# Performance work log

Measured on AMD Instinct MI355X. Metric: run time of the kernel, lower is better.

The kernel has to match this reference:

```python
import jax, jax.numpy as jnp
import numpy as np

N_HEAD = 16
N_KV_HEAD = 4
WINDOW = 256
ROPE_BASE = 10000.0


def _rotate_half(x):
    h = x.shape[-1] // 2
    return jnp.concatenate([-x[..., h:], x[..., :h]], axis=-1)


def _rope_cos_sin(T, D):
    inv_freq = 1.0 / (ROPE_BASE ** (jnp.arange(0, D, 2, dtype=jnp.float32) / D))
    t = jnp.arange(T, dtype=jnp.float32)
    freqs = t[:, None] * inv_freq[None, :]            # [T, D/2]
    emb = jnp.concatenate([freqs, freqs], axis=-1)    # [T, D]
    return jnp.cos(emb)[None, None], jnp.sin(emb)[None, None]  # [1,1,T,D]


def _masks(T, w):
    tq = jnp.arange(T)
    tk = jnp.arange(T)
    causal = tk[None, :] <= tq[:, None]
    i_blk = (tq // w) * w                              # window block start per query
    k_start = jnp.maximum(0, i_blk - w // 2)           # local key slice start
    # torch SDPA is_causal with L!=S: top-left aligned tril -> local kj <= local qi
    upper = tq - (i_blk - k_start)
    local = (tk[None, :] >= k_start[:, None]) & (tk[None, :] <= upper[:, None])
    return causal, local


def setup_inputs() -> dict:
    key = jax.random.key(0)
    k0, k1, k2, k3, k4 = jax.random.split(key, 5)
    B, T, C = 1, 2048, 2048
    D = C // N_HEAD
    s = 0.02
    return {
        "x": jax.random.normal(k0, (B, T, C), dtype=jnp.float32),
        "wq": jax.random.normal(k1, (C, N_HEAD * D), dtype=jnp.float32) * s,
        "wk": jax.random.normal(k2, (C, N_KV_HEAD * D), dtype=jnp.float32) * s,
        "wv": jax.random.normal(k3, (C, N_KV_HEAD * D), dtype=jnp.float32) * s,
        "wo": jax.random.normal(k4, (C, C), dtype=jnp.float32) * s,
    }


def reference(x, wq, wk, wv, wo):
    B, T, C = x.shape
    D = C // N_HEAD
    g = N_HEAD // N_KV_HEAD

    q = (x @ wq).reshape(B, T, N_HEAD, D)
    k = (x @ wk).reshape(B, T, N_KV_HEAD, D)
    v = (x @ wv).reshape(B, T, N_KV_HEAD, D)
    k = jnp.repeat(k, g, axis=2)                       # GQA repeat_interleave
    v = jnp.repeat(v, g, axis=2)
    q = q.transpose(0, 2, 1, 3)                        # [B,H,T,D]
    k = k.transpose(0, 2, 1, 3)
    v = v.transpose(0, 2, 1, 3)

    cos, sin = _rope_cos_sin(T, D)
    q = q * cos + _rotate_half(q) * sin
    k = k * cos + _rotate_half(k) * sin

    scale = 1.0 / jnp.sqrt(jnp.asarray(D, dtype=q.dtype))
    scores = jnp.einsum('bhqd,bhkd->bhqk', q, k) * scale
    causal, local = _masks(T, WINDOW)
    neg = jnp.finfo(scores.dtype).min
    p_g = jax.nn.softmax(jnp.where(causal, scores, neg), axis=-1)
    p_l = jax.nn.softmax(jnp.where(local, scores, neg), axis=-1)
    out_g = jnp.einsum('bhqk,bhkd->bhqd', p_g, v)
    out_l = jnp.einsum('bhqk,bhkd->bhqd', p_l, v)
    out = 0.5 * (out_g + out_l)
    out = out.transpose(0, 2, 1, 3).reshape(B, T, C)
    return out @ wo
```

## Files before the change

### kernel.cpp

```cpp
#include <hip/hip_runtime.h>
#include <hip/hip_bf16.h>
#include <cstdint>
#include <cstddef>

#define T_SEQ 2048
#define CDIM  2048
#define HQ    16
#define HKV   4
#define DHEAD 128
#define NQKV  3072

typedef __bf16 bf8 __attribute__((ext_vector_type(8)));
typedef __bf16 bf4 __attribute__((ext_vector_type(4)));
typedef float  f4  __attribute__((ext_vector_type(4)));

static __device__ __forceinline__ f4 mfma16(bf8 a, bf8 b, f4 c) {
    return __builtin_amdgcn_mfma_f32_16x16x32_bf16(a, b, c, 0, 0, 0);
}

#define GLOAD16(g, l)                                                        \
    __builtin_amdgcn_global_load_lds(                                        \
        (const __attribute__((address_space(1))) void*)(g),                  \
        (__attribute__((address_space(3))) void*)(l), 16, 0, 0)

__global__ __launch_bounds__(256) void k_prep(const float* __restrict__ in,
                                              __bf16* __restrict__ out,
                                              float* __restrict__ tab) {
    const int bid = blockIdx.x;
    if (bid < 4096) {
        int i = bid * 256 + threadIdx.x;
        float4 v = ((const float4*)in)[i];
        bf4 o;
        o[0] = (__bf16)v.x; o[1] = (__bf16)v.y; o[2] = (__bf16)v.z; o[3] = (__bf16)v.w;
        ((bf4*)out)[i] = o;
    } else {
        int idx = (bid - 4096) * 256 + threadIdx.x;
        int t = idx >> 6, j = idx & 63;
        float invf = expf(-(float)j * (9.210340371976184f / 64.0f));
        float a = (float)t * invf;
        tab[idx * 2 + 0] = cosf(a);
        tab[idx * 2 + 1] = sinf(a);
    }
}

__global__ __launch_bounds__(256) void k_tpose4(const float* __restrict__ wq,
                                                const float* __restrict__ wk,
                                                const float* __restrict__ wv,
                                                const float* __restrict__ wo,
                                                __bf16* __restrict__ wqkvT,
                                                __bf16* __restrict__ woT) {
    __shared__ float tile[32][33];
    const int bx = blockIdx.x;
    const float* src; __bf16* dst; int ld_src, cx;
    if (bx < 64)      { src = wq; dst = wqkvT;                        ld_src = 2048; cx = bx; }
    else if (bx < 80) { src = wk; dst = wqkvT + (size_t)2048 * 2048;  ld_src = 512;  cx = bx - 64; }
    else if (bx < 96) { src = wv; dst = wqkvT + (size_t)2560 * 2048;  ld_src = 512;  cx = bx - 80; }
    else              { src = wo; dst = woT;                          ld_src = 2048; cx = bx - 96; }
    const int c0 = cx * 32, r0 = blockIdx.y * 32;
    const int tx = threadIdx.x, ty = threadIdx.y;
#pragma unroll
    for (int i = 0; i < 4; ++i)
        tile[ty + i * 8][tx] = src[(size_t)(r0 + ty + i * 8) * ld_src + c0 + tx];
    __syncthreads();
#pragma unroll
    for (int i = 0; i < 4; ++i)
        dst[(size_t)(c0 + ty + i * 8) * 2048 + r0 + tx] = (__bf16)tile[tx][ty + i * 8];
}

template <int MODE>
__global__ __launch_bounds__(256, 2) void k_gemm(const __bf16* __restrict__ A,
                                                 const __bf16* __restrict__ BT,
                                                 float* __restrict__ C,
                                                 const float2* __restrict__ tab,
                                                 __bf16* __restrict__ Qo,
                                                 __bf16* __restrict__ Ko,
                                                 __bf16* __restrict__ Vo,
                                                 int M, int N, int K) {
    __shared__ __bf16 lds[2][2][128 * 64];
    char* L = (char*)&lds[0][0][0];
    const int tid = threadIdx.x, wid = tid >> 6, lane = tid & 63;
    const int l15 = lane & 15, lhi = lane >> 4;
    const int wr = wid >> 1, wc = wid & 1;
    const size_t arow0 = (size_t)blockIdx.y * 128;
    const size_t brow0 = (size_t)blockIdx.x * 128;

    const int sr = tid >> 3;
    const int sc8 = ((tid & 7) ^ ((tid >> 3) & 7)) * 8;
    const __bf16* Ag = A + (arow0 + sr) * K + sc8;
    const __bf16* Bg = BT + (brow0 + sr) * K + sc8;

#define GSTAGE(buf, k0)                                                          \
    {                                                                            \
        _Pragma("unroll") for (int i = 0; i < 4; ++i) {                          \
            GLOAD16(Ag + (k0) + (size_t)i * 32 * K,                              \
                    L + (buf) * 32768 + i * 4096 + tid * 16);                    \
            GLOAD16(Bg + (k0) + (size_t)i * 32 * K,                              \
                    L + (buf) * 32768 + 16384 + i * 4096 + tid * 16);            \
        }                                                                        \
    }

    f4 acc[4][4] = {};
    GSTAGE(0, 0);
    __syncthreads();
    int cur = 0;

    for (int k0 = 0; k0 < K; k0 += 64) {
        if (k0 + 64 < K) GSTAGE(cur ^ 1, k0 + 64);
        const char* Ab = L + cur * 32768;
        const char* Bb = Ab + 16384;
        bf8 af[2][4], bfr[2][4];
#pragma unroll
        for (int kk = 0; kk < 2; ++kk) {
            const int ch = ((kk * 4 + lhi) ^ (l15 & 7)) * 16;
#pragma unroll
            for (int m = 0; m < 4; ++m)
                af[kk][m] = *(const bf8*)(Ab + (wr * 64 + m * 16 + l15) * 128 + ch);
#pragma unroll
            for (int n = 0; n < 4; ++n)
                bfr[kk][n] = *(const bf8*)(Bb + (n * 32 + wc * 16 + l15) * 128 + ch);
        }
        __builtin_amdgcn_s_setprio(1);
#pragma unroll
        for (int kk = 0; kk < 2; ++kk)
#pragma unroll
            for (int m = 0; m < 4; ++m)
#pragma unroll
                for (int n = 0; n < 4; ++n)
                    acc[m][n] = mfma16(af[kk][m], bfr[kk][n], acc[m][n]);
        __builtin_amdgcn_s_setprio(0);
        __syncthreads();
        cur ^= 1;
    }
#undef GSTAGE

    const int row0 = blockIdx.y * 128 + wr * 64;
    if (MODE == 0) {
#pragma unroll
        for (int m = 0; m < 4; ++m)
#pragma unroll
            for (int n = 0; n < 4; ++n) {
                const int c = blockIdx.x * 128 + n * 32 + wc * 16 + l15;
#pragma unroll
                for (int j = 0; j < 4; ++j)
                    C[(size_t)(row0 + m * 16 + lhi * 4 + j) * N + c] = acc[m][n][j];
            }
    } else {
        const int bx = blockIdx.x;
        if (bx < 20) {
            __bf16* dst0 = (bx < 16) ? (Qo + (size_t)bx * T_SEQ * DHEAD)
                                     : (Ko + (size_t)(bx - 16) * T_SEQ * DHEAD);
#pragma unroll
            for (int m = 0; m < 4; ++m)
#pragma unroll
                for (int n = 0; n < 2; ++n) {
                    const int d = n * 32 + wc * 16 + l15;
#pragma unroll
                    for (int j = 0; j < 4; ++j) {
                        const int t = row0 + m * 16 + lhi * 4 + j;
                        const float2 cs = tab[t * 64 + d];
                        const float a = acc[m][n][j], b = acc[m][n + 2][j];
                        dst0[(size_t)t * DHEAD + d]      = (__bf16)(a * cs.x - b * cs.y);
                        dst0[(size_t)t * DHEAD + d + 64] = (__bf16)(b * cs.x + a * cs.y);
                    }
                }
        } else {
            __bf16* vdst = Vo + (size_t)(bx - 20) * DHEAD * T_SEQ;
#pragma unroll
            for (int m = 0; m < 4; ++m)
#pragma unroll
                for (int n = 0; n < 4; ++n) {
                    const int c = n * 32 + wc * 16 + l15;
                    bf4 o;
#pragma unroll
                    for (int j = 0; j < 4; ++j) o[j] = (__bf16)acc[m][n][j];
                    *(bf4*)&vdst[(size_t)c * T_SEQ + row0 + m * 16 + lhi * 4] = o;
                }
        }
    }
}

__global__ __launch_bounds__(512) void k_attn(const __bf16* __restrict__ Q,
                                              const __bf16* __restrict__ Kr,
                                              const __bf16* __restrict__ VT,
                                              __bf16* __restrict__ att) {
    __shared__ __align__(16) char lds[155648];
    char* KlB  = lds;
    char* VlB  = lds + 65536;
    char* PlB0 = lds + 131072;
    char* PwB0 = lds + 147456;

    const int h = blockIdx.y, kvh = h >> 2;
    const int qt = (blockIdx.y < 8) ? (31 - (int)blockIdx.x) : (int)blockIdx.x;
    const int tid = threadIdx.x, wid = tid >> 6, lane = tid & 63;
    const int l15 = lane & 15, lhi = lane >> 4;
    const int par = wid >> 2, qw = wid & 3;
    const int q0w = qt * 64 + qw * 16;
    const bool hasloc = qt >= 4;
    const int lfLo = 4 * (qt >> 2) - 2;
    const int lpart = qt - 2;
    const float CE = 0.12751741f;
    const float L2E = 1.44269504f;
    const float SCL = 0.08838834764831845f;
    const float THR = 5.5451774f;

    char* PlB = PlB0 + wid * 2048;
    char* PwB = PwB0 + qw * 2048;

    const int srow = tid >> 4;
    const int sg = (((tid & 15) ^ (srow & 15)) << 3);
    const __bf16* KgB = Kr + (size_t)kvh * T_SEQ * DHEAD;
    const __bf16* VgB = VT + (size_t)kvh * DHEAD * T_SEQ;

#define STAGE(bsel, kb2)                                                          \
    {                                                                             \
        _Pragma("unroll") for (int i = 0; i < 4; ++i) {                           \
            GLOAD16(KgB + (size_t)((kb2) + i * 32 + srow) * DHEAD + sg,           \
                    KlB + (bsel) + i * 8192 + tid * 16);                          \
            GLOAD16(VgB + (size_t)(i * 32 + srow) * T_SEQ + (kb2) + sg,           \
                    VlB + (bsel) + i * 8192 + tid * 16);                          \
        }                                                                         \
    }

    bf8 qf[4];
#pragma unroll
    for (int dc = 0; dc < 4; ++dc)
        qf[dc] = *(const bf8*)&Q[((size_t)h * T_SEQ + q0w + l15) * DHEAD + dc * 32 + lhi * 8];

    f4 oc[8] = {}, ow[8] = {};
    float mg[4], sgp[4], slp[4];
#pragma unroll
    for (int j = 0; j < 4; ++j) { mg[j] = -__builtin_inff(); sgp[j] = slp[j] = 0.f; }
    float mgmin = -__builtin_inff();

    const int R = (qt >> 1) + 1;
    STAGE(0, 0);
    __syncthreads();
    int cur = 0;

    for (int r = 0; r < R; ++r) {
        if (r + 1 < R) STAGE((cur ^ 1) * 32768, (r + 1) * 128);
        const int kt = 2 * r + par;
        if (kt <= qt) {
            const int kb = kt * 64;
            const int cb = cur * 32768;
            const int rowb = par * 64;
            f4 sc[4] = {};
            __builtin_amdgcn_s_setprio(1);
#pragma unroll
            for (int ks = 0; ks < 4; ++ks)
#pragma unroll
                for (int dc = 0; dc < 4; ++dc) {
                    bf8 kf = *(const bf8*)(KlB + cb + (rowb + ks * 16 + l15) * 256 +
                                           (((dc * 4 + lhi) ^ l15) << 4));
                    sc[ks] = mfma16(qf[dc], kf, sc[ks]);
                }
            __builtin_amdgcn_s_setprio(0);

            float t[4][4];
#pragma unroll
            for (int ks = 0; ks < 4; ++ks)
#pragma unroll
                for (int j = 0; j < 4; ++j) t[ks][j] = sc[ks][j];
            if (kt == qt) {
#pragma unroll
                for (int ks = 0; ks < 4; ++ks)
#pragma unroll
                    for (int j = 0; j < 4; ++j)
                        if (kb + ks * 16 + l15 > q0w + lhi * 4 + j) t[ks][j] = -3.0e38f;
            }
            float mx = t[0][0];
#pragma unroll
            for (int ks = 0; ks < 4; ++ks)
#pragma unroll
                for (int j = 0; j < 4; ++j) mx = fmaxf(mx, t[ks][j]);
            mx *= SCL;
            if (!__all(mx <= mgmin + THR)) {
#pragma unroll
                for (int j = 0; j < 4; ++j) {
                    float m2 = fmaxf(fmaxf(t[0][j], t[1][j]), fmaxf(t[2][j], t[3][j])) * SCL;
#pragma unroll
                    for (int x = 1; x < 16; x <<= 1) m2 = fmaxf(m2, __shfl_xor(m2, x));
                    float mn = fmaxf(mg[j], m2);
                    float f = __builtin_amdgcn_exp2f((mg[j] - mn) * L2E);
                    mg[j] = mn;
                    sgp[j] *= f; slp[j] *= f;
#pragma unroll
                    for (int nd = 0; nd < 8; ++nd) { oc[nd][j] *= f; ow[nd][j] *= f; }
                }
                mgmin = fminf(fminf(mg[0], mg[1]), fminf(mg[2], mg[3]));
            }
            float p[4][4], psum[4];
#pragma unroll
            for (int j = 0; j < 4; ++j) {
                const float bj = mg[j] * L2E;
#pragma unroll
                for (int ks = 0; ks < 4; ++ks)
                    p[ks][j] = __builtin_amdgcn_exp2f(t[ks][j] * CE - bj);
                psum[j] = (p[0][j] + p[1][j]) + (p[2][j] + p[3][j]);
                sgp[j] += psum[j];
            }
            const bool part = hasloc && (kt == lpart);
            if (!part) {
#pragma unroll
                for (int j = 0; j < 4; ++j) {
                    const int rsw = ((lhi * 4 + j) & 7) << 4;
                    const int rb = (lhi * 4 + j) * 128;
#pragma unroll
                    for (int ks = 0; ks < 4; ++ks)
                        *(__bf16*)(PlB + rb + ((ks * 32 + 2 * l15) ^ rsw)) = (__bf16)p[ks][j];
                }
            } else {
                const int e = q0w + lhi * 4 - 128 - kb - l15;
#pragma unroll
                for (int j = 0; j < 4; ++j) {
                    const int rsw = ((lhi * 4 + j) & 7) << 4;
                    const int rb = (lhi * 4 + j) * 128;
                    float lsum = 0.f;
#pragma unroll
                    for (int ks = 0; ks < 4; ++ks) {
                        float l = (ks * 16 <= e + j) ? p[ks][j] : 0.f;
                        lsum += l;
                        *(__bf16*)(PwB + rb + ((ks * 32 + 2 * l15) ^ rsw)) = (__bf16)l;
                        *(__bf16*)(PlB + rb + ((ks * 32 + 2 * l15) ^ rsw)) = (__bf16)(p[ks][j] - l);
                    }
                    slp[j] += lsum;
                }
            }
            const bool inwin = hasloc && kt >= lfLo && kt < lpart;
            if (inwin) {
#pragma unroll
                for (int j = 0; j < 4; ++j) slp[j] += psum[j];
            }
            const int psw = (l15 & 7) << 4;
            bf8 pf0 = *(const bf8*)(PlB + l15 * 128 + ((lhi << 4) ^ psw));
            bf8 pf1 = *(const bf8*)(PlB + l15 * 128 + ((64 + (lhi << 4)) ^ psw));
            const int vg0 = ((par * 8 + lhi) ^ l15) << 4;
            const int vg1 = ((par * 8 + 4 + lhi) ^ l15) << 4;
            __builtin_amdgcn_s_setprio(1);
            if (part) {
                bf8 pw0 = *(const bf8*)(PwB + l15 * 128 + ((lhi << 4) ^ psw));
                bf8 pw1 = *(const bf8*)(PwB + l15 * 128 + ((64 + (lhi << 4)) ^ psw));
#pragma unroll
                for (int nd = 0; nd < 8; ++nd) {
                    bf8 v0 = *(const bf8*)(VlB + cb + (nd * 16 + l15) * 256 + vg0);
                    bf8 v1 = *(const bf8*)(VlB + cb + (nd * 16 + l15) * 256 + vg1);
                    oc[nd] = mfma16(pf0, v0, oc[nd]);
                    oc[nd] = mfma16(pf1, v1, oc[nd]);
                    ow[nd] = mfma16(pw0, v0, ow[nd]);
                    ow[nd] = mfma16(pw1, v1, ow[nd]);
                }
            } else if (inwin) {
#pragma unroll
                for (int nd = 0; nd < 8; ++nd) {
                    bf8 v0 = *(const bf8*)(VlB + cb + (nd * 16 + l15) * 256 + vg0);
                    bf8 v1 = *(const bf8*)(VlB + cb + (nd * 16 + l15) * 256 + vg1);
                    ow[nd] = mfma16(pf0, v0, ow[nd]);
                    ow[nd] = mfma16(pf1, v1, ow[nd]);
                }
            } else {
#pragma unroll
                for (int nd = 0; nd < 8; ++nd) {
                    bf8 v0 = *(const bf8*)(VlB + cb + (nd * 16 + l15) * 256 + vg0);
                    bf8 v1 = *(const bf8*)(VlB + cb + (nd * 16 + l15) * 256 + vg1);
                    oc[nd] = mfma16(pf0, v0, oc[nd]);
                    oc[nd] = mfma16(pf1, v1, oc[nd]);
                }
            }
            __builtin_amdgcn_s_setprio(0);
        }
        __syncthreads();
        cur ^= 1;
    }

    if (par) {
        char* sb = lds + qw * 20480 + lane * 320;
#pragma unroll
        for (int nd = 0; nd < 8; ++nd) *(f4*)(sb + nd * 16) = oc[nd];
#pragma unroll
        for (int nd = 0; nd < 8; ++nd) *(f4*)(sb + 128 + nd * 16) = ow[nd];
        f4 a, b, c;
#pragma unroll
        for (int j = 0; j < 4; ++j) { a[j] = mg[j]; b[j] = sgp[j]; c[j] = slp[j]; }
        *(f4*)(sb + 256) = a; *(f4*)(sb + 272) = b; *(f4*)(sb + 288) = c;
    }
    __syncthreads();
    if (!par) {
        char* sb = lds + qw * 20480 + lane * 320;
        f4 mB = *(const f4*)(sb + 256);
        f4 sB = *(const f4*)(sb + 272);
        f4 lB = *(const f4*)(sb + 288);
        float fA[4], fB[4];
#pragma unroll
        for (int j = 0; j < 4; ++j) {
            float ms = fmaxf(mg[j], mB[j]);
            fA[j] = __builtin_amdgcn_exp2f((mg[j] - ms) * L2E);
            fB[j] = __builtin_amdgcn_exp2f((mB[j] - ms) * L2E);
            sgp[j] = sgp[j] * fA[j] + sB[j] * fB[j];
            slp[j] = slp[j] * fA[j] + lB[j] * fB[j];
        }
#pragma unroll
        for (int nd = 0; nd < 8; ++nd) {
            f4 ocB = *(const f4*)(sb + nd * 16);
            f4 owB = *(const f4*)(sb + 128 + nd * 16);
#pragma unroll
            for (int j = 0; j < 4; ++j) {
                oc[nd][j] = oc[nd][j] * fA[j] + ocB[j] * fB[j];
                ow[nd][j] = ow[nd][j] * fA[j] + owB[j] * fB[j];
            }
        }
#pragma unroll
        for (int j = 0; j < 4; ++j) {
#pragma unroll
            for (int x = 1; x < 16; x <<= 1) {
                sgp[j] += __shfl_xor(sgp[j], x);
                slp[j] += __shfl_xor(slp[j], x);
            }
        }
        float rg[4], rl[4];
#pragma unroll
        for (int j = 0; j < 4; ++j) {
            rg[j] = 1.f / sgp[j];
            rl[j] = hasloc ? 0.5f / slp[j] : 0.f;
        }
#pragma unroll
        for (int nd = 0; nd < 8; ++nd)
#pragma unroll
            for (int j = 0; j < 4; ++j) {
                int q = q0w + lhi * 4 + j;
                float go = oc[nd][j] + ow[nd][j];
                float v = hasloc ? (go * (0.5f * rg[j]) + ow[nd][j] * rl[j]) : go * rg[j];
                att[(size_t)q * CDIM + h * DHEAD + nd * 16 + l15] = (__bf16)v;
            }
    }
#undef STAGE
}

extern "C" void kernel_launch(void* const* d_in, const int* in_sizes, int n_in,
                              void* d_out, int out_size, void* d_ws, size_t ws_size,
                              hipStream_t stream) {
    const float* x  = (const float*)d_in[0];
    const float* wq = (const float*)d_in[1];
    const float* wk = (const float*)d_in[2];
    const float* wv = (const float*)d_in[3];
    const float* wo = (const float*)d_in[4];
    char* ws = (char*)d_ws;

    __bf16* xbf   = (__bf16*)(ws + 0);
    __bf16* wqkvT = (__bf16*)(ws + 8388608);
    __bf16* woT   = (__bf16*)(ws + 20971520);
    __bf16* Q     = (__bf16*)(ws + 41943040);
    __bf16* K     = (__bf16*)(ws + 50331648);
    __bf16* VTb   = (__bf16*)(ws + 52428800);
    __bf16* att   = (__bf16*)(ws + 54525952);
    float*  tab   = (float*)(ws + 62914560);

    k_prep<<<4608, 256, 0, stream>>>(x, xbf, tab);
    k_tpose4<<<dim3(160, 64), dim3(32, 8), 0, stream>>>(wq, wk, wv, wo, wqkvT, woT);
    k_gemm<1><<<dim3(24, 16), 256, 0, stream>>>(xbf, wqkvT, nullptr, (const float2*)tab,
                                                Q, K, VTb, 2048, 3072, 2048);
    k_attn<<<dim3(32, 16), 512, 0, stream>>>(Q, K, VTb, att);
    k_gemm<0><<<dim3(16, 16), 256, 0, stream>>>(att, woT, (float*)d_out, nullptr,
                                                nullptr, nullptr, nullptr, 2048, 2048, 2048);
}
```

Measured before the change: 140.2 us.

## Use eight waves per GEMM tile and merge prep and weight-transpose kernels

The GEMM block grows from 256 to 512 threads. Each of the eight waves now computes a 32x64 sub-tile of the 128x128 output instead of 64x64, and the global-to-LDS staging loop is reshaped to match. The aim is to raise waves per CU and hide more latency, since the grids are small relative to the CU count; the cost is fewer MFMAs per LDS fragment load per wave. Separately, the x/bf16 conversion, RoPE table and weight transpose kernels become one launch with block-index dispatch, removing a kernel launch and its gap.

Measured after the change: 138.1 us, median of 2. No clear change (-1.5%).

```diff
diff --git a/kernel.cpp b/kernel.cpp
--- a/kernel.cpp
+++ b/kernel.cpp
@@ -23,41 +23,43 @@
         (const __attribute__((address_space(1))) void*)(g),                  \
         (__attribute__((address_space(3))) void*)(l), 16, 0, 0)
 
-__global__ __launch_bounds__(256) void k_prep(const float* __restrict__ in,
-                                              __bf16* __restrict__ out,
-                                              float* __restrict__ tab) {
-    const int bid = blockIdx.x;
+__global__ __launch_bounds__(256) void k_pre(const float* __restrict__ x,
+                                             const float* __restrict__ wq,
+                                             const float* __restrict__ wk,
+                                             const float* __restrict__ wv,
+                                             const float* __restrict__ wo,
+                                             __bf16* __restrict__ xbf,
+                                             float* __restrict__ tab,
+                                             __bf16* __restrict__ wqkvT,
+                                             __bf16* __restrict__ woT) {
+    const int bid = blockIdx.x, tid = threadIdx.x;
     if (bid < 4096) {
-        int i = bid * 256 + threadIdx.x;
-        float4 v = ((const float4*)in)[i];
+        int i = bid * 256 + tid;
+        float4 v = ((const float4*)x)[i];
         bf4 o;
         o[0] = (__bf16)v.x; o[1] = (__bf16)v.y; o[2] = (__bf16)v.z; o[3] = (__bf16)v.w;
-        ((bf4*)out)[i] = o;
-    } else {
-        int idx = (bid - 4096) * 256 + threadIdx.x;
+        ((bf4*)xbf)[i] = o;
+        return;
+    }
+    if (bid < 4608) {
+        int idx = (bid - 4096) * 256 + tid;
         int t = idx >> 6, j = idx & 63;
         float invf = expf(-(float)j * (9.210340371976184f / 64.0f));
         float a = (float)t * invf;
         tab[idx * 2 + 0] = cosf(a);
         tab[idx * 2 + 1] = sinf(a);
-    }
-}
-
-__global__ __launch_bounds__(256) void k_tpose4(const float* __restrict__ wq,
-                                                const float* __restrict__ wk,
-                                                const float* __restrict__ wv,
-                                                const float* __restrict__ wo,
-                                                __bf16* __restrict__ wqkvT,
-                                                __bf16* __restrict__ woT) {
+        return;
+    }
     __shared__ float tile[32][33];
-    const int bx = blockIdx.x;
+    const int n = bid - 4608;
+    const int bx = n % 160, by = n / 160;
     const float* src; __bf16* dst; int ld_src, cx;
     if (bx < 64)      { src = wq; dst = wqkvT;                        ld_src = 2048; cx = bx; }
     else if (bx < 80) { src = wk; dst = wqkvT + (size_t)2048 * 2048;  ld_src = 512;  cx = bx - 64; }
     else if (bx < 96) { src = wv; dst = wqkvT + (size_t)2560 * 2048;  ld_src = 512;  cx = bx - 80; }
     else              { src = wo; dst = woT;                          ld_src = 2048; cx = bx - 96; }
-    const int c0 = cx * 32, r0 = blockIdx.y * 32;
-    const int tx = threadIdx.x, ty = threadIdx.y;
+    const int c0 = cx * 32, r0 = by * 32;
+    const int tx = tid & 31, ty = tid >> 5;
 #pragma unroll
     for (int i = 0; i < 4; ++i)
         tile[ty + i * 8][tx] = src[(size_t)(r0 + ty + i * 8) * ld_src + c0 + tx];
@@ -68,7 +70,7 @@
 }
 
 template <int MODE>
-__global__ __launch_bounds__(256, 2) void k_gemm(const __bf16* __restrict__ A,
+__global__ __launch_bounds__(512, 4) void k_gemm(const __bf16* __restrict__ A,
                                                  const __bf16* __restrict__ BT,
                                                  float* __restrict__ C,
                                                  const float2* __restrict__ tab,
@@ -91,15 +93,15 @@
 
 #define GSTAGE(buf, k0)                                                          \
     {                                                                            \
-        _Pragma("unroll") for (int i = 0; i < 4; ++i) {                          \
-            GLOAD16(Ag + (k0) + (size_t)i * 32 * K,                              \
-                    L + (buf) * 32768 + i * 4096 + tid * 16);                    \
-            GLOAD16(Bg + (k0) + (size_t)i * 32 * K,                              \
-                    L + (buf) * 32768 + 16384 + i * 4096 + tid * 16);            \
+        _Pragma("unroll") for (int i = 0; i < 2; ++i) {                          \
+            GLOAD16(Ag + (k0) + (size_t)i * 64 * K,                              \
+                    L + (buf) * 32768 + i * 8192 + tid * 16);                    \
+            GLOAD16(Bg + (k0) + (size_t)i * 64 * K,                              \
+                    L + (buf) * 32768 + 16384 + i * 8192 + tid * 16);            \
         }                                                                        \
     }
 
-    f4 acc[4][4] = {};
+    f4 acc[2][4] = {};
     GSTAGE(0, 0);
     __syncthreads();
     int cur = 0;
@@ -108,13 +110,13 @@
         if (k0 + 64 < K) GSTAGE(cur ^ 1, k0 + 64);
         const char* Ab = L + cur * 32768;
         const char* Bb = Ab + 16384;
-        bf8 af[2][4], bfr[2][4];
+        bf8 af[2][2], bfr[2][4];
 #pragma unroll
         for (int kk = 0; kk < 2; ++kk) {
             const int ch = ((kk * 4 + lhi) ^ (l15 & 7)) * 16;
 #pragma unroll
-            for (int m = 0; m < 4; ++m)
-                af[kk][m] = *(const bf8*)(Ab + (wr * 64 + m * 16 + l15) * 128 + ch);
+            for (int m = 0; m < 2; ++m)
+                af[kk][m] = *(const bf8*)(Ab + (wr * 32 + m * 16 + l15) * 128 + ch);
 #pragma unroll
             for (int n = 0; n < 4; ++n)
                 bfr[kk][n] = *(const bf8*)(Bb + (n * 32 + wc * 16 + l15) * 128 + ch);
@@ -123,7 +125,7 @@
 #pragma unroll
         for (int kk = 0; kk < 2; ++kk)
 #pragma unroll
-            for (int m = 0; m < 4; ++m)
+            for (int m = 0; m < 2; ++m)
 #pragma unroll
                 for (int n = 0; n < 4; ++n)
                     acc[m][n] = mfma16(af[kk][m], bfr[kk][n], acc[m][n]);
@@ -133,10 +135,10 @@
     }
 #undef GSTAGE
 
-    const int row0 = blockIdx.y * 128 + wr * 64;
+    const int row0 = blockIdx.y * 128 + wr * 32;
     if (MODE == 0) {
 #pragma unroll
-        for (int m = 0; m < 4; ++m)
+        for (int m = 0; m < 2; ++m)
 #pragma unroll
             for (int n = 0; n < 4; ++n) {
                 const int c = blockIdx.x * 128 + n * 32 + wc * 16 + l15;
@@ -150,7 +152,7 @@
             __bf16* dst0 = (bx < 16) ? (Qo + (size_t)bx * T_SEQ * DHEAD)
                                      : (Ko + (size_t)(bx - 16) * T_SEQ * DHEAD);
 #pragma unroll
-            for (int m = 0; m < 4; ++m)
+            for (int m = 0; m < 2; ++m)
 #pragma unroll
                 for (int n = 0; n < 2; ++n) {
                     const int d = n * 32 + wc * 16 + l15;
@@ -166,7 +168,7 @@
         } else {
             __bf16* vdst = Vo + (size_t)(bx - 20) * DHEAD * T_SEQ;
 #pragma unroll
-            for (int m = 0; m < 4; ++m)
+            for (int m = 0; m < 2; ++m)
 #pragma unroll
                 for (int n = 0; n < 4; ++n) {
                     const int c = n * 32 + wc * 16 + l15;
@@ -454,11 +456,10 @@
     __bf16* att   = (__bf16*)(ws + 54525952);
     float*  tab   = (float*)(ws + 62914560);
 
-    k_prep<<<4608, 256, 0, stream>>>(x, xbf, tab);
-    k_tpose4<<<dim3(160, 64), dim3(32, 8), 0, stream>>>(wq, wk, wv, wo, wqkvT, woT);
-    k_gemm<1><<<dim3(24, 16), 256, 0, stream>>>(xbf, wqkvT, nullptr, (const float2*)tab,
+    k_pre<<<14848, 256, 0, stream>>>(x, wq, wk, wv, wo, xbf, tab, wqkvT, woT);
+    k_gemm<1><<<dim3(24, 16), 512, 0, stream>>>(xbf, wqkvT, nullptr, (const float2*)tab,
                                                 Q, K, VTb, 2048, 3072, 2048);
     k_attn<<<dim3(32, 16), 512, 0, stream>>>(Q, K, VTb, att);
-    k_gemm<0><<<dim3(16, 16), 256, 0, stream>>>(att, woT, (float*)d_out, nullptr,
+    k_gemm<0><<<dim3(16, 16), 512, 0, stream>>>(att, woT, (float*)d_out, nullptr,
                                                 nullptr, nullptr, nullptr, 2048, 2048, 2048);
 }
```
